# Kernel optimization log

Measured on AMD Instinct MI355X. Metric: run time of the kernel, lower is better.

The kernel has to match this reference:

```python
import jax, jax.numpy as jnp
import numpy as np

N_NODES = 89250


def gcn_conv(x, W, b, src, dst, n):
    # h = X W  (dense transform before aggregation, as in PyG GCNConv)
    h = x @ W
    # add self loops
    loop = jnp.arange(n, dtype=src.dtype)
    src_all = jnp.concatenate([src, loop])
    dst_all = jnp.concatenate([dst, loop])
    # symmetric degree normalization D^-1/2 A_hat D^-1/2 (degree from targets)
    deg = jax.ops.segment_sum(jnp.ones_like(dst_all, dtype=h.dtype), dst_all, num_segments=n)
    dinv = jnp.where(deg > 0, jax.lax.rsqrt(deg), 0.0)
    norm = dinv[src_all] * dinv[dst_all]  # [E+n]
    # gather source features, scale, scatter-add to targets
    msg = h[src_all] * norm[:, None]
    out = jax.ops.segment_sum(msg, dst_all, num_segments=n)
    return out + b


def setup_inputs() -> dict:
    key = jax.random.key(0)
    k1, k2, k3, k4, k5 = jax.random.split(key, 5)
    n, f, h, c, e = N_NODES, 500, 64, 7, 899756
    x = jax.random.normal(k1, (n, f), dtype=jnp.float32)
    edge_index = jax.random.randint(k2, (2, e), 0, n, dtype=jnp.int64)
    W1 = jax.random.normal(k3, (f, h), dtype=jnp.float32) / np.sqrt(f)
    b1 = jnp.zeros((h,), dtype=jnp.float32)
    W2 = jax.random.normal(k4, (h, c), dtype=jnp.float32) / np.sqrt(h)
    b2 = jnp.zeros((c,), dtype=jnp.float32)
    return {"x": x, "W1": W1, "b1": b1, "W2": W2, "b2": b2, "edge_index": edge_index}


def reference(x, W1, b1, W2, b2, edge_index):
    n = x.shape[0]
    src, dst = edge_index[0], edge_index[1]
    h = jax.nn.relu(gcn_conv(x, W1, b1, src, dst, n))
    out = gcn_conv(h, W2, b2, src, dst, n)
    return out
```

## Files before the change

### kernel.cpp

```cpp
#include <hip/hip_runtime.h>
#include <cstdint>

#define F_IN 500
#define HID  64
#define NCLS 7
#define KCH  100
#define XS_STRIDE 108

static inline size_t align_up(size_t v, size_t a) { return (v + a - 1) & ~(a - 1); }

__global__ void hist_kernel(const int* __restrict__ dst, int* __restrict__ hist, int E) {
    int i = blockIdx.x * blockDim.x + threadIdx.x;
    if (i < E) atomicAdd(&hist[dst[i]], 1);
}

__global__ void dinv_kernel(const int* __restrict__ hist, float* __restrict__ dinv, int n) {
    int i = blockIdx.x * blockDim.x + threadIdx.x;
    if (i < n) dinv[i] = rsqrtf((float)hist[i] + 1.0f);
}

__global__ __launch_bounds__(256) void scan1_kernel(const int* __restrict__ hist,
                                                    int* __restrict__ rowstart,
                                                    int* __restrict__ bsum, int n) {
    __shared__ int sdat[256];
    int tid = threadIdx.x;
    int i = blockIdx.x * 256 + tid;
    int v = (i < n) ? hist[i] : 0;
    sdat[tid] = v;
    __syncthreads();
    for (int off = 1; off < 256; off <<= 1) {
        int t = (tid >= off) ? sdat[tid - off] : 0;
        __syncthreads();
        sdat[tid] += t;
        __syncthreads();
    }
    int incl = sdat[tid];
    if (i < n) rowstart[i] = incl - v;
    if (tid == 255) bsum[blockIdx.x] = incl;
}

__global__ __launch_bounds__(512) void scan2_kernel(int* __restrict__ bsum, int nb) {
    __shared__ int sdat[512];
    int tid = threadIdx.x;
    int v = (tid < nb) ? bsum[tid] : 0;
    sdat[tid] = v;
    __syncthreads();
    for (int off = 1; off < 512; off <<= 1) {
        int t = (tid >= off) ? sdat[tid - off] : 0;
        __syncthreads();
        sdat[tid] += t;
        __syncthreads();
    }
    bsum[tid] = sdat[tid] - v;
}

__global__ void scan3_kernel(int* __restrict__ rowstart, const int* __restrict__ bsum,
                             int* __restrict__ cursor, int n, int E) {
    int i = blockIdx.x * blockDim.x + threadIdx.x;
    if (i < n) {
        int val = rowstart[i] + bsum[i >> 8];
        rowstart[i] = val;
        cursor[i] = val;
    }
    if (i == 0) rowstart[n] = E;
}

__global__ void scatter_kernel(const int* __restrict__ src, const int* __restrict__ dst,
                               int* __restrict__ cursor, int* __restrict__ csrc, int E) {
    int e = blockIdx.x * blockDim.x + threadIdx.x;
    if (e < E) {
        int d = dst[e];
        int pos = atomicAdd(&cursor[d], 1);
        csrc[pos] = src[e];
    }
}

__global__ __launch_bounds__(256) void gemm1_kernel(
    const float* __restrict__ x, const float* __restrict__ W1,
    float* __restrict__ h0, int n)
{
    __shared__ float Xs[64 * XS_STRIDE];
    __shared__ float Ws[KCH * HID];

    const int tid  = threadIdx.x;
    const int col4 = (tid & 15) * 4;
    const int row4 = (tid >> 4) * 4;
    const int row0 = blockIdx.x * 64;

    float acc[4][4];
    #pragma unroll
    for (int r = 0; r < 4; ++r)
        #pragma unroll
        for (int c = 0; c < 4; ++c) acc[r][c] = 0.f;

    for (int kc = 0; kc < 5; ++kc) {
        const int kbase = kc * KCH;
        __syncthreads();
        for (int f = tid; f < 64 * 25; f += 256) {
            int r  = f / 25;
            int c4 = f - r * 25;
            int row = row0 + r;
            row = (row < n) ? row : (n - 1);
            float4 v = *reinterpret_cast<const float4*>(x + (size_t)row * F_IN + kbase + c4 * 4);
            *reinterpret_cast<float4*>(&Xs[r * XS_STRIDE + c4 * 4]) = v;
        }
        for (int f = tid; f < KCH * 16; f += 256) {
            int k  = f >> 4;
            int c4 = f & 15;
            float4 v = *reinterpret_cast<const float4*>(W1 + (size_t)(kbase + k) * HID + c4 * 4);
            *reinterpret_cast<float4*>(&Ws[k * HID + c4 * 4]) = v;
        }
        __syncthreads();

        for (int k4 = 0; k4 < KCH / 4; ++k4) {
            float4 Xv[4], Wv[4];
            #pragma unroll
            for (int r = 0; r < 4; ++r)
                Xv[r] = *reinterpret_cast<const float4*>(&Xs[(row4 + r) * XS_STRIDE + k4 * 4]);
            #pragma unroll
            for (int j = 0; j < 4; ++j)
                Wv[j] = *reinterpret_cast<const float4*>(&Ws[(k4 * 4 + j) * HID + col4]);
            #pragma unroll
            for (int r = 0; r < 4; ++r) {
                acc[r][0] = fmaf(Xv[r].x, Wv[0].x, acc[r][0]);
                acc[r][1] = fmaf(Xv[r].x, Wv[0].y, acc[r][1]);
                acc[r][2] = fmaf(Xv[r].x, Wv[0].z, acc[r][2]);
                acc[r][3] = fmaf(Xv[r].x, Wv[0].w, acc[r][3]);
                acc[r][0] = fmaf(Xv[r].y, Wv[1].x, acc[r][0]);
                acc[r][1] = fmaf(Xv[r].y, Wv[1].y, acc[r][1]);
                acc[r][2] = fmaf(Xv[r].y, Wv[1].z, acc[r][2]);
                acc[r][3] = fmaf(Xv[r].y, Wv[1].w, acc[r][3]);
                acc[r][0] = fmaf(Xv[r].z, Wv[2].x, acc[r][0]);
                acc[r][1] = fmaf(Xv[r].z, Wv[2].y, acc[r][1]);
                acc[r][2] = fmaf(Xv[r].z, Wv[2].z, acc[r][2]);
                acc[r][3] = fmaf(Xv[r].z, Wv[2].w, acc[r][3]);
                acc[r][0] = fmaf(Xv[r].w, Wv[3].x, acc[r][0]);
                acc[r][1] = fmaf(Xv[r].w, Wv[3].y, acc[r][1]);
                acc[r][2] = fmaf(Xv[r].w, Wv[3].z, acc[r][2]);
                acc[r][3] = fmaf(Xv[r].w, Wv[3].w, acc[r][3]);
            }
        }
    }

    #pragma unroll
    for (int r = 0; r < 4; ++r) {
        int row = row0 + row4 + r;
        if (row < n) {
            float4 v = make_float4(acc[r][0], acc[r][1], acc[r][2], acc[r][3]);
            *reinterpret_cast<float4*>(h0 + (size_t)row * HID + col4) = v;
        }
    }
}

__global__ __launch_bounds__(256) void agg1_gemm2_kernel(
    const float* __restrict__ h0, const float* __restrict__ dinv,
    const int* __restrict__ rowstart, const int* __restrict__ csrc,
    const float* __restrict__ b1, const float* __restrict__ W2,
    float* __restrict__ h2, int n)
{
    __shared__ float W2s[HID][9];
    __shared__ float b1s[HID];
    for (int i = threadIdx.x; i < HID * 8; i += 256) {
        int k = i >> 3, c = i & 7;
        W2s[k][c] = (c < NCLS) ? W2[k * NCLS + c] : 0.f;
    }
    if (threadIdx.x < HID) b1s[threadIdx.x] = b1[threadIdx.x];
    __syncthreads();

    const int lane = threadIdx.x & 63;
    const int wave = threadIdx.x >> 6;
    const int d = blockIdx.x * 4 + wave;
    if (d >= n) return;

    const int js = rowstart[d];
    const int je = rowstart[d + 1];
    float acc = 0.f;
    for (int j = js; j < je; ++j) {
        int s = csrc[j];
        acc = fmaf(h0[(size_t)s * HID + lane], dinv[s], acc);
    }
    const float dd = dinv[d];
    float v = (acc + dd * h0[(size_t)d * HID + lane]) * dd;
    float p = fmaxf(v + b1s[lane], 0.f);

    float t0 = p * W2s[lane][0];
    float t1 = p * W2s[lane][1];
    float t2 = p * W2s[lane][2];
    float t3 = p * W2s[lane][3];
    float t4 = p * W2s[lane][4];
    float t5 = p * W2s[lane][5];
    float t6 = p * W2s[lane][6];
    #pragma unroll
    for (int off = 32; off > 0; off >>= 1) {
        t0 += __shfl_xor(t0, off);
        t1 += __shfl_xor(t1, off);
        t2 += __shfl_xor(t2, off);
        t3 += __shfl_xor(t3, off);
        t4 += __shfl_xor(t4, off);
        t5 += __shfl_xor(t5, off);
        t6 += __shfl_xor(t6, off);
    }
    float sel = t0;
    sel = (lane == 1) ? t1 : sel;
    sel = (lane == 2) ? t2 : sel;
    sel = (lane == 3) ? t3 : sel;
    sel = (lane == 4) ? t4 : sel;
    sel = (lane == 5) ? t5 : sel;
    sel = (lane == 6) ? t6 : sel;
    if (lane < NCLS) h2[(size_t)d * 8 + lane] = sel;
}

__global__ void agg2_kernel(const float* __restrict__ h2, const float* __restrict__ dinv,
                            const int* __restrict__ rowstart, const int* __restrict__ csrc,
                            const float* __restrict__ b2, float* __restrict__ out, int n)
{
    int idx = blockIdx.x * blockDim.x + threadIdx.x;
    int d = idx >> 3;
    int c = idx & 7;
    if (d >= n) return;

    const int js = rowstart[d];
    const int je = rowstart[d + 1];
    float acc = 0.f;
    for (int j = js; j < je; ++j) {
        int s = csrc[j];
        acc = fmaf(h2[(size_t)s * 8 + c], dinv[s], acc);
    }
    const float dd = dinv[d];
    if (c < NCLS)
        out[(size_t)d * NCLS + c] = fmaf(acc + dd * h2[(size_t)d * 8 + c], dd, b2[c]);
}

extern "C" void kernel_launch(void* const* d_in, const int* in_sizes, int n_in,
                              void* d_out, int out_size, void* d_ws, size_t ws_size,
                              hipStream_t stream)
{
    const float* x  = (const float*)d_in[0];
    const float* W1 = (const float*)d_in[1];
    const float* b1 = (const float*)d_in[2];
    const float* W2 = (const float*)d_in[3];
    const float* b2 = (const float*)d_in[4];
    const int*   ei = (const int*)d_in[5];

    const int n = in_sizes[0] / F_IN;
    const int E = in_sizes[5] / 2;
    const int* src = ei;
    const int* dst = ei + E;

    char* ws = (char*)d_ws;
    size_t off = 0;
    int*   hist     = (int*)(ws + off);   off += align_up((size_t)n * 4, 256);
    int*   rowstart = (int*)(ws + off);   off += align_up((size_t)(n + 1) * 4, 256);
    int*   bsum     = (int*)(ws + off);   off += align_up((size_t)512 * 4, 256);
    int*   csrc     = (int*)(ws + off);   off += align_up((size_t)E * 4, 256);
    float* dinv     = (float*)(ws + off); off += align_up((size_t)n * 4, 256);
    float* h0       = (float*)(ws + off); off += align_up((size_t)n * HID * 4, 256);
    float* h2       = (float*)(ws + off); off += align_up((size_t)n * 8 * 4, 256);
    float* out      = (float*)d_out;

    const int nb = (n + 255) / 256;

    hipMemsetAsync(hist, 0, (size_t)n * 4, stream);
    hist_kernel<<<(E + 255) / 256, 256, 0, stream>>>(dst, hist, E);
    dinv_kernel<<<nb, 256, 0, stream>>>(hist, dinv, n);
    scan1_kernel<<<nb, 256, 0, stream>>>(hist, rowstart, bsum, n);
    scan2_kernel<<<1, 512, 0, stream>>>(bsum, nb);
    scan3_kernel<<<nb, 256, 0, stream>>>(rowstart, bsum, hist , n, E);
    scatter_kernel<<<(E + 255) / 256, 256, 0, stream>>>(src, dst, hist , csrc, E);

    gemm1_kernel<<<(n + 63) / 64, 256, 0, stream>>>(x, W1, h0, n);

    agg1_gemm2_kernel<<<(n + 3) / 4, 256, 0, stream>>>(h0, dinv, rowstart, csrc, b1, W2, h2, n);

    agg2_kernel<<<((size_t)n * 8 + 255) / 256, 256, 0, stream>>>(h2, dinv, rowstart, csrc, b2, out, n);
}
```

Before: 563.3 us.

## Replace FP32 SIMT first-layer GEMM with bf16 MFMA kernel

Replaces the FP32 FMA-based X·W1 GEMM with a bf16 MFMA (16x16x32) kernel using 128-row tiles. X is converted to bf16 on the fly while staging into LDS, and a new small kernel pre-transposes and converts W1 to bf16, padded to K=512. The aim is to move the dense transform from vector ALUs onto matrix cores. The cost is reduced precision in the first layer and an extra kernel launch. The GEMM still has to read 178MB of fp32 X, so it remains bandwidth-bound.

```diff
diff --git a/kernel.cpp b/kernel.cpp
--- a/kernel.cpp
+++ b/kernel.cpp
@@ -4,10 +4,20 @@
 #define F_IN 500
 #define HID  64
 #define NCLS 7
-#define KCH  100
-#define XS_STRIDE 108
+
+typedef __attribute__((ext_vector_type(8))) short v8s;
+typedef __attribute__((ext_vector_type(4))) short v4s;
+typedef __attribute__((ext_vector_type(4))) float v4f;
+
+union S8 { v8s v; v4s h[2]; };
 
 static inline size_t align_up(size_t v, size_t a) { return (v + a - 1) & ~(a - 1); }
+
+__device__ inline unsigned short f2bf(float f) {
+    unsigned int u = __float_as_uint(f);
+    u += 0x7FFF + ((u >> 16) & 1);
+    return (unsigned short)(u >> 16);
+}
 
 __global__ void hist_kernel(const int* __restrict__ dst, int* __restrict__ hist, int E) {
     int i = blockIdx.x * blockDim.x + threadIdx.x;
@@ -75,79 +85,98 @@
     }
 }
 
-__global__ __launch_bounds__(256) void gemm1_kernel(
-    const float* __restrict__ x, const float* __restrict__ W1,
+__global__ void wt_kernel(const float* __restrict__ W1, unsigned short* __restrict__ Wt) {
+    int id = blockIdx.x * 256 + threadIdx.x;
+    if (id >= HID * 512) return;
+    int c = id >> 9;
+    int k = id & 511;
+    Wt[(size_t)c * 512 + k] = (k < F_IN) ? f2bf(W1[(size_t)k * HID + c]) : (unsigned short)0;
+}
+
+__global__ __launch_bounds__(256) void gemm1_mfma_kernel(
+    const float* __restrict__ x, const unsigned short* __restrict__ Wt,
     float* __restrict__ h0, int n)
 {
-    __shared__ float Xs[64 * XS_STRIDE];
-    __shared__ float Ws[KCH * HID];
+    __shared__ unsigned short Al[128][36];
+    __shared__ unsigned short Bl[64][36];
 
     const int tid  = threadIdx.x;
-    const int col4 = (tid & 15) * 4;
-    const int row4 = (tid >> 4) * 4;
-    const int row0 = blockIdx.x * 64;
-
-    float acc[4][4];
+    const int lane = tid & 63;
+    const int wave = tid >> 6;
+    const int row0 = blockIdx.x * 128;
+    const int l15  = lane & 15;
+    const int kq   = (lane >> 4) * 4;
+
+    v4f acc[2][4];
     #pragma unroll
-    for (int r = 0; r < 4; ++r)
-        #pragma unroll
-        for (int c = 0; c < 4; ++c) acc[r][c] = 0.f;
-
-    for (int kc = 0; kc < 5; ++kc) {
-        const int kbase = kc * KCH;
-        __syncthreads();
-        for (int f = tid; f < 64 * 25; f += 256) {
-            int r  = f / 25;
-            int c4 = f - r * 25;
+    for (int rb = 0; rb < 2; ++rb)
+        #pragma unroll
+        for (int cb = 0; cb < 4; ++cb) acc[rb][cb] = (v4f)(0.0f);
+
+    const int a_c4 = tid & 7;
+    const int a_r  = tid >> 3;
+    const int b_c  = tid >> 2;
+    const int b_k8 = (tid & 3) * 8;
+
+    for (int ks = 0; ks < 16; ++ks) {
+        const int kbase = ks * 32;
+        __syncthreads();
+        #pragma unroll
+        for (int i = 0; i < 4; ++i) {
+            const int r = a_r + 32 * i;
             int row = row0 + r;
             row = (row < n) ? row : (n - 1);
-            float4 v = *reinterpret_cast<const float4*>(x + (size_t)row * F_IN + kbase + c4 * 4);
-            *reinterpret_cast<float4*>(&Xs[r * XS_STRIDE + c4 * 4]) = v;
-        }
-        for (int f = tid; f < KCH * 16; f += 256) {
-            int k  = f >> 4;
-            int c4 = f & 15;
-            float4 v = *reinterpret_cast<const float4*>(W1 + (size_t)(kbase + k) * HID + c4 * 4);
-            *reinterpret_cast<float4*>(&Ws[k * HID + c4 * 4]) = v;
-        }
-        __syncthreads();
-
-        for (int k4 = 0; k4 < KCH / 4; ++k4) {
-            float4 Xv[4], Wv[4];
+            v4s o;
+            if (kbase + a_c4 * 4 < F_IN) {
+                float4 v = *reinterpret_cast<const float4*>(
+                    x + (size_t)row * F_IN + kbase + a_c4 * 4);
+                o.x = (short)f2bf(v.x); o.y = (short)f2bf(v.y);
+                o.z = (short)f2bf(v.z); o.w = (short)f2bf(v.w);
+            } else {
+                o = (v4s)(short)0;
+            }
+            *reinterpret_cast<v4s*>(&Al[r][a_c4 * 4]) = o;
+        }
+        {
+            const unsigned short* p = Wt + (size_t)b_c * 512 + kbase + b_k8;
+            v4s lo = *reinterpret_cast<const v4s*>(p);
+            v4s hi = *reinterpret_cast<const v4s*>(p + 4);
+            *reinterpret_cast<v4s*>(&Bl[b_c][b_k8])     = lo;
+            *reinterpret_cast<v4s*>(&Bl[b_c][b_k8 + 4]) = hi;
+        }
+        __syncthreads();
+
+        S8 af[2], bq[4];
+        #pragma unroll
+        for (int rb = 0; rb < 2; ++rb) {
+            const int row = wave * 32 + rb * 16 + l15;
+            af[rb].h[0] = *reinterpret_cast<const v4s*>(&Al[row][kq]);
+            af[rb].h[1] = *reinterpret_cast<const v4s*>(&Al[row][kq + 16]);
+        }
+        #pragma unroll
+        for (int cb = 0; cb < 4; ++cb) {
+            const int col = cb * 16 + l15;
+            bq[cb].h[0] = *reinterpret_cast<const v4s*>(&Bl[col][kq]);
+            bq[cb].h[1] = *reinterpret_cast<const v4s*>(&Bl[col][kq + 16]);
+        }
+        #pragma unroll
+        for (int rb = 0; rb < 2; ++rb)
             #pragma unroll
-            for (int r = 0; r < 4; ++r)
-                Xv[r] = *reinterpret_cast<const float4*>(&Xs[(row4 + r) * XS_STRIDE + k4 * 4]);
+            for (int cb = 0; cb < 4; ++cb)
+                acc[rb][cb] = __builtin_amdgcn_mfma_f32_16x16x32_bf16(
+                    af[rb].v, bq[cb].v, acc[rb][cb], 0, 0, 0);
+    }
+
+    #pragma unroll
+    for (int rb = 0; rb < 2; ++rb) {
+        #pragma unroll
+        for (int cb = 0; cb < 4; ++cb) {
             #pragma unroll
-            for (int j = 0; j < 4; ++j)
-                Wv[j] = *reinterpret_cast<const float4*>(&Ws[(k4 * 4 + j) * HID + col4]);
-            #pragma unroll
-            for (int r = 0; r < 4; ++r) {
-                acc[r][0] = fmaf(Xv[r].x, Wv[0].x, acc[r][0]);
-                acc[r][1] = fmaf(Xv[r].x, Wv[0].y, acc[r][1]);
-                acc[r][2] = fmaf(Xv[r].x, Wv[0].z, acc[r][2]);
-                acc[r][3] = fmaf(Xv[r].x, Wv[0].w, acc[r][3]);
-                acc[r][0] = fmaf(Xv[r].y, Wv[1].x, acc[r][0]);
-                acc[r][1] = fmaf(Xv[r].y, Wv[1].y, acc[r][1]);
-                acc[r][2] = fmaf(Xv[r].y, Wv[1].z, acc[r][2]);
-                acc[r][3] = fmaf(Xv[r].y, Wv[1].w, acc[r][3]);
-                acc[r][0] = fmaf(Xv[r].z, Wv[2].x, acc[r][0]);
-                acc[r][1] = fmaf(Xv[r].z, Wv[2].y, acc[r][1]);
-                acc[r][2] = fmaf(Xv[r].z, Wv[2].z, acc[r][2]);
-                acc[r][3] = fmaf(Xv[r].z, Wv[2].w, acc[r][3]);
-                acc[r][0] = fmaf(Xv[r].w, Wv[3].x, acc[r][0]);
-                acc[r][1] = fmaf(Xv[r].w, Wv[3].y, acc[r][1]);
-                acc[r][2] = fmaf(Xv[r].w, Wv[3].z, acc[r][2]);
-                acc[r][3] = fmaf(Xv[r].w, Wv[3].w, acc[r][3]);
+            for (int j = 0; j < 4; ++j) {
+                int row = row0 + wave * 32 + rb * 16 + (lane >> 4) * 4 + j;
+                if (row < n)
+                    h0[(size_t)row * HID + cb * 16 + l15] = acc[rb][cb][j];
             }
-        }
-    }
-
-    #pragma unroll
-    for (int r = 0; r < 4; ++r) {
-        int row = row0 + row4 + r;
-        if (row < n) {
-            float4 v = make_float4(acc[r][0], acc[r][1], acc[r][2], acc[r][3]);
-            *reinterpret_cast<float4*>(h0 + (size_t)row * HID + col4) = v;
         }
     }
 }
@@ -256,6 +285,7 @@
     float* dinv     = (float*)(ws + off); off += align_up((size_t)n * 4, 256);
     float* h0       = (float*)(ws + off); off += align_up((size_t)n * HID * 4, 256);
     float* h2       = (float*)(ws + off); off += align_up((size_t)n * 8 * 4, 256);
+    unsigned short* Wt = (unsigned short*)(ws + off); off += align_up((size_t)HID * 512 * 2, 256);
     float* out      = (float*)d_out;
 
     const int nb = (n + 255) / 256;
@@ -268,7 +298,8 @@
     scan3_kernel<<<nb, 256, 0, stream>>>(rowstart, bsum, hist , n, E);
     scatter_kernel<<<(E + 255) / 256, 256, 0, stream>>>(src, dst, hist , csrc, E);
 
-    gemm1_kernel<<<(n + 63) / 64, 256, 0, stream>>>(x, W1, h0, n);
+    wt_kernel<<<(HID * 512 + 255) / 256, 256, 0, stream>>>(W1, Wt);
+    gemm1_mfma_kernel<<<(n + 127) / 128, 256, 0, stream>>>(x, Wt, h0, n);
 
     agg1_gemm2_kernel<<<(n + 3) / 4, 256, 0, stream>>>(h0, dinv, rowstart, csrc, b1, W2, h2, n);
 
```

New measurement: 503.9 us. -10.5%, faster.
